# Optimization experiments

Measured on AMD Instinct MI355X. Metric: run time of the kernel, lower is better.

The kernel has to match this reference:

```python
import jax, jax.numpy as jnp
import numpy as np

RC = 6.0
N_BASIS = 32
WIDTH = 0.25
N_CONV = 3
MU = jnp.linspace(0.5, 6.0, N_BASIS)  # Gaussian RBF centers ('distances')


def ssp(x):
    # shifted softplus activation (SchNet-style)
    return jax.nn.softplus(x) - jnp.log(2.0)


def setup_inputs() -> dict:
    key = jax.random.key(0)
    ks = jax.random.split(key, 20)
    B, N, F, K = 16, 128, 128, 32
    S = 16  # n_species
    coords = jax.random.normal(ks[0], (B, N, 3), dtype=jnp.float32) * 4.0
    species = jax.random.randint(ks[1], (B, N), 0, S)
    g = lambda k, shape, fan: jax.random.normal(k, shape, dtype=jnp.float32) / np.sqrt(fan)
    return {
        "coords": coords,
        "species": species,
        "emb_table": g(ks[2], (S, F), 1.0),
        # convolve_net: K -> F -> F
        "Wc1": g(ks[3], (K, F), K), "bc1": jnp.zeros((F,)),
        "Wc2": g(ks[4], (F, F), F), "bc2": jnp.zeros((F,)),
        # update_net: F -> F -> F
        "Wu1": g(ks[5], (F, F), F), "bu1": jnp.zeros((F,)),
        "Wu2": g(ks[6], (F, F), F), "bu2": jnp.zeros((F,)),
        # pool_net: F -> 64 -> 8 (isotropic coefficients)
        "Wp1": g(ks[7], (F, 64), F), "bp1": jnp.zeros((64,)),
        "Wp2": g(ks[8], (64, 8), 64), "bp2": jnp.zeros((8,)),
        # edge_net: 2F -> F -> 16 (anisotropic coefficients); split as Wi/Wj
        "Wei": g(ks[9], (F, F), 2 * F), "Wej": g(ks[10], (F, F), 2 * F),
        "be1": jnp.zeros((F,)),
        "We2": g(ks[11], (F, 16), F), "be2": jnp.zeros((16,)),
    }


def reference(coords, species, emb_table,
              Wc1, bc1, Wc2, bc2,
              Wu1, bu1, Wu2, bu2,
              Wp1, bp1, Wp2, bp2,
              Wei, Wej, be1, We2, be2):
    B, N, _ = coords.shape
    # --- MolecularEmbedding ---
    h = emb_table[species]                                   # [B,N,F]
    # --- pairwise geometry (shared across conv iterations; coords fixed) ---
    diff = coords[:, :, None, :] - coords[:, None, :, :]      # [B,N,N,3]
    d2 = jnp.sum(diff * diff, axis=-1)                        # [B,N,N]
    d = jnp.sqrt(jnp.where(d2 > 0, d2, 1.0))                  # safe sqrt (diag masked out)
    eye = jnp.eye(N, dtype=bool)
    mask = ((d < RC) & ~eye).astype(h.dtype)[..., None]       # [B,N,N,1]
    rbf = jnp.exp(-((d[..., None] - MU) ** 2) / (2.0 * WIDTH ** 2))  # [B,N,N,K]
    # convolve_net: RBF -> continuous filter weights [B,N,N,F]
    Wf = (ssp(rbf @ Wc1 + bc1) @ Wc2 + bc2) * mask
    # --- n_convolutions x MessagePassing ---
    for _ in range(N_CONV):
        m = jnp.einsum('bijf,bjf->bif', Wf, h)                # gather-weight-scatter
        h = h + (ssp(m @ Wu1 + bu1) @ Wu2 + bu2)              # update_net (residual)
    # --- NodePool -> c_iso [B,N,8] ---
    c_iso = ssp(h @ Wp1 + bp1) @ Wp2 + bp2
    # --- EdgePool -> c_aniso [B,N,N,16], summed over neighbor axis ---
    pre_i = h @ Wei                                           # [B,N,F]
    pre_j = h @ Wej                                           # [B,N,F]
    hid = ssp(pre_i[:, :, None, :] + pre_j[:, None, :, :] + be1)  # [B,N,N,F]
    c_aniso = (hid @ We2 + be2) * mask                        # [B,N,N,16]
    return c_iso, c_aniso.sum(2)
```

## Files before the change

### kernel.cpp

```cpp
#include <hip/hip_runtime.h>


#define LN2F 0.69314718055994531f

__device__ __forceinline__ float sspf(float x) {
  float e = __expf(-fabsf(x));
  return fmaxf(x, 0.0f) + __logf(1.0f + e) - LN2F;
}
__device__ __forceinline__ unsigned int f2bf(float x) {
  unsigned int u = __float_as_uint(x);
  return (u + 0x7fffu + ((u >> 16) & 1u)) >> 16;
}
__device__ __forceinline__ float bflo(unsigned int u) { return __uint_as_float(u << 16); }
__device__ __forceinline__ float bfhi(unsigned int u) { return __uint_as_float(u & 0xffff0000u); }

__global__ __launch_bounds__(256) void prep_kernel(
    const float* __restrict__ coords,
    const float* __restrict__ Wc1, const float* __restrict__ bc1,
    const float* __restrict__ Wc2, const float* __restrict__ bc2,
    float* __restrict__ table,
    unsigned int* __restrict__ ent, int* __restrict__ cnt) {
  int t = threadIdx.x;
  if (blockIdx.x < 1024) {
    __shared__ int wc[4];
    int node = blockIdx.x * 2 + (t >> 7);
    int j = t & 127;
    int b = node >> 7, i = node & 127;
    const float* cb = coords + (b << 7) * 3;
    float dx = cb[i*3+0] - cb[j*3+0];
    float dy = cb[i*3+1] - cb[j*3+1];
    float dz = cb[i*3+2] - cb[j*3+2];
    float d  = sqrtf(dx*dx + dy*dy + dz*dz);
    bool valid = (d < 6.0f) && (j != i);
    int k = 4096;
    if (valid) { k = (int)(d * (4096.0f/6.0f)); if (k > 4095) k = 4095; }
    unsigned long long bal = __ballot(valid);
    int lane = t & 63, w = t >> 6;
    if (lane == 0) wc[w] = (int)__popcll(bal);
    __syncthreads();
    int ii = t >> 7;
    int nn = wc[2*ii] + wc[2*ii+1];
    int base = ((w & 1) ? wc[w-1] : 0) + (int)__popcll(bal & ((1ull << lane) - 1ull));
    if (valid) ent[node*128 + base] = (unsigned int)(j | (k << 7));
    int nnp = (nn + 3) & ~3;
    if (j >= nn && j < nnp) ent[node*128 + j] = (4096u << 7);
    if (j == 0) cnt[node] = nn | (nnp << 16);
  } else {
    __shared__ float rbf[8][32];
    __shared__ float hid[8][128];
    int tb = (int)blockIdx.x - 1024;
    int t0 = tb * 8;
    { int tt = t >> 5, kk = t & 31;
      float d = (float)(t0 + tt) * (6.0f/4096.0f) + 0.5f * (6.0f/4096.0f);
      float mu = 0.5f + (float)kk * (5.5f/31.0f);
      float z = d - mu;
      rbf[tt][kk] = __expf(-8.0f * z * z); }
    __syncthreads();
    int f = t & 127, sub = t >> 7;
    float s0 = bc1[f], s1 = s0, s2 = s0, s3 = s0;
    int r0 = sub * 4;
    for (int kk = 0; kk < 32; kk++) {
      float wv = Wc1[kk*128 + f];
      s0 += rbf[r0+0][kk]*wv; s1 += rbf[r0+1][kk]*wv;
      s2 += rbf[r0+2][kk]*wv; s3 += rbf[r0+3][kk]*wv;
    }
    hid[r0+0][f] = sspf(s0); hid[r0+1][f] = sspf(s1);
    hid[r0+2][f] = sspf(s2); hid[r0+3][f] = sspf(s3);
    __syncthreads();
    float o0 = bc2[f], o1 = o0, o2 = o0, o3 = o0;
    for (int g = 0; g < 128; g++) {
      float wv = Wc2[g*128 + f];
      o0 += hid[r0+0][g]*wv; o1 += hid[r0+1][g]*wv;
      o2 += hid[r0+2][g]*wv; o3 += hid[r0+3][g]*wv;
    }
    table[(t0+r0+0)*128 + f] = o0;
    table[(t0+r0+1)*128 + f] = o1;
    table[(t0+r0+2)*128 + f] = o2;
    table[(t0+r0+3)*128 + f] = o3;
    if (tb == 0 && t < 128) table[4096*128 + t] = 0.0f;
  }
}

template<bool SRC_EMB, bool LAST>
__global__ __launch_bounds__(512) void conv_t(
    const float* __restrict__ h_in, const unsigned int* __restrict__ hbf_in,
    float* __restrict__ h_out, unsigned int* __restrict__ hbf_out,
    const int* __restrict__ species, const float* __restrict__ emb,
    const float* __restrict__ table, const unsigned int* __restrict__ ent,
    const int* __restrict__ cnt,
    const float* __restrict__ Wu1, const float* __restrict__ bu1,
    const float* __restrict__ Wu2, const float* __restrict__ bu2,
    const float* __restrict__ Wp1, const float* __restrict__ bp1,
    const float* __restrict__ Wp2, const float* __restrict__ bp2,
    const float* __restrict__ Wei, const float* __restrict__ Wej,
    float* __restrict__ pre_i, unsigned int* __restrict__ prejbf,
    float* __restrict__ out) {
  __shared__ unsigned int hsh[8192];
  __shared__ unsigned int ent_s[4][128];
  __shared__ float mred[8][128];
  __shared__ float m_s[4][128];
  __shared__ float red[4][4][128];
  __shared__ float u1_s[4][128];
  __shared__ int nn_s[4];
  int t = threadIdx.x;
  int node0 = blockIdx.x * 4;
  int b = blockIdx.x >> 5;

  if constexpr (SRC_EMB) {
    const int* spb = species + (b << 7);
    for (int c = 0; c < 16; c++) {
      int idx = c*512 + t;
      int j = idx >> 6, f2 = idx & 63;
      float2 v = *(const float2*)(emb + spb[j]*128 + 2*f2);
      hsh[idx] = (f2bf(v.y) << 16) | f2bf(v.x);
    }
  } else {
    const unsigned int* hb = hbf_in + b * 8192;
    for (int c = 0; c < 16; c++) hsh[c*512 + t] = hb[c*512 + t];
  }
  { int ii = t >> 7, f = t & 127;
    ent_s[ii][f] = ent[(node0 + ii)*128 + f]; }
  if (t < 4) nn_s[t] = cnt[node0 + t];
  __syncthreads();

  int w = t >> 6, lane = t & 63;
  int ii = w >> 1, par = w & 1;
  int nnp = nn_s[ii] >> 16;
  float a0 = 0.f, a1 = 0.f, c0 = 0.f, c1 = 0.f;
  for (int e = par; e + 2 < nnp; e += 4) {
    unsigned int u0 = ent_s[ii][e], u1 = ent_s[ii][e + 2];
    int j0 = u0 & 127, k0 = (int)(u0 >> 7);
    int j1 = u1 & 127, k1 = (int)(u1 >> 7);
    float2 t0 = *(const float2*)(table + k0*128 + 2*lane);
    float2 t1 = *(const float2*)(table + k1*128 + 2*lane);
    unsigned int h0 = hsh[j0*64 + lane];
    unsigned int h1 = hsh[j1*64 + lane];
    a0 += t0.x * bflo(h0); a1 += t0.y * bfhi(h0);
    c0 += t1.x * bflo(h1); c1 += t1.y * bfhi(h1);
  }
  a0 += c0; a1 += c1;
  *(float2*)&mred[w][2*lane] = make_float2(a0, a1);
  __syncthreads();
  { int i2 = t >> 7, f = t & 127;
    m_s[i2][f] = mred[2*i2][f] + mred[2*i2+1][f]; }
  __syncthreads();

  int g = t & 127, q = t >> 7;
  {
    float p0=0,p1=0,p2=0,p3=0;
    for (int f = q*32; f < q*32 + 32; f++) {
      float wv = Wu1[f*128 + g];
      p0 += m_s[0][f]*wv; p1 += m_s[1][f]*wv; p2 += m_s[2][f]*wv; p3 += m_s[3][f]*wv;
    }
    red[q][0][g]=p0; red[q][1][g]=p1; red[q][2][g]=p2; red[q][3][g]=p3;
  }
  __syncthreads();
  { int i2 = t >> 7, gg = t & 127;
    u1_s[i2][gg] = sspf(red[0][i2][gg]+red[1][i2][gg]+red[2][i2][gg]+red[3][i2][gg] + bu1[gg]); }
  __syncthreads();
  {
    float p0=0,p1=0,p2=0,p3=0;
    for (int f = q*32; f < q*32 + 32; f++) {
      float wv = Wu2[f*128 + g];
      p0 += u1_s[0][f]*wv; p1 += u1_s[1][f]*wv; p2 += u1_s[2][f]*wv; p3 += u1_s[3][f]*wv;
    }
    red[q][0][g]=p0; red[q][1][g]=p1; red[q][2][g]=p2; red[q][3][g]=p3;
  }
  __syncthreads();
  { int i2 = t >> 7, o = t & 127;
    int node = node0 + i2;
    float delta = red[0][i2][o]+red[1][i2][o]+red[2][i2][o]+red[3][i2][o] + bu2[o];
    float base;
    if constexpr (SRC_EMB) base = emb[species[node]*128 + o];
    else                   base = h_in[node*128 + o];
    float hf = base + delta;
    if constexpr (!LAST) {
      h_out[node*128 + o] = hf;
      unsigned int lo = f2bf(hf);
      unsigned int hi = (unsigned int)__shfl_xor((int)lo, 1);
      if ((o & 1) == 0) hbf_out[node*64 + (o >> 1)] = lo | (hi << 16);
    } else {
      u1_s[i2][o] = hf;
    }
  }
  if constexpr (LAST) {
    __syncthreads();
    float (*hs)[128]     = u1_s;
    float (*redp)[4][64] = reinterpret_cast<float (*)[4][64]>(red);
    float (*us)[64]      = reinterpret_cast<float (*)[64]>(m_s);
    int gp = t & 63, qp = t >> 6;
    float p0=0,p1=0,p2=0,p3=0;
    for (int f = qp*16; f < qp*16 + 16; f++) {
      float wv = Wp1[f*64 + gp];
      p0 += hs[0][f]*wv; p1 += hs[1][f]*wv; p2 += hs[2][f]*wv; p3 += hs[3][f]*wv;
    }
    redp[qp][0][gp]=p0; redp[qp][1][gp]=p1; redp[qp][2][gp]=p2; redp[qp][3][gp]=p3;
    __syncthreads();
    if (t < 256) {
      int i4 = t >> 6, gg = t & 63;
      float s = bp1[gg];
      for (int q2 = 0; q2 < 8; q2++) s += redp[q2][i4][gg];
      us[i4][gg] = sspf(s);
    }
    __syncthreads();
    if (t < 32) {
      int i4 = t >> 3, o = t & 7;
      float v = bp2[o];
      for (int gg = 0; gg < 64; gg++) v += us[i4][gg] * Wp2[gg*8 + o];
      out[(node0 + i4)*8 + o] = v;
    }
    int o = t & 127, sel = (t >> 7) & 1, duo = t >> 8;
    const float* W = sel ? Wej : Wei;
    float q0 = 0.f, q1 = 0.f;
    for (int f = 0; f < 128; f++) {
      float wv = W[f*128 + o];
      q0 += hs[2*duo][f]*wv; q1 += hs[2*duo+1][f]*wv;
    }
    if (sel == 0) {
      pre_i[(node0 + 2*duo)*128 + o]     = q0;
      pre_i[(node0 + 2*duo + 1)*128 + o] = q1;
    } else {
      unsigned int l0 = f2bf(q0), l1 = f2bf(q1);
      unsigned int h0 = (unsigned int)__shfl_xor((int)l0, 1);
      unsigned int h1 = (unsigned int)__shfl_xor((int)l1, 1);
      if ((o & 1) == 0) {
        prejbf[(node0 + 2*duo)*64 + (o >> 1)]     = l0 | (h0 << 16);
        prejbf[(node0 + 2*duo + 1)*64 + (o >> 1)] = l1 | (h1 << 16);
      }
    }
  }
}

__global__ __launch_bounds__(512) void edgepool_kernel(
    const float* __restrict__ pre_i, const unsigned int* __restrict__ prejbf,
    const unsigned int* __restrict__ ent, const int* __restrict__ cnt,
    const float* __restrict__ be1, const float* __restrict__ We2,
    const float* __restrict__ be2, float* __restrict__ out) {
  __shared__ unsigned int pjs[8192];
  __shared__ unsigned int ent_s[4][128];
  __shared__ float pis[4][128];
  __shared__ float sred[8][128];
  __shared__ float s_s[4][128];
  __shared__ float r2[4][8][16];
  __shared__ int nn_s[4];
  int t = threadIdx.x;
  int node0 = blockIdx.x * 4;
  int b = blockIdx.x >> 5;
  const unsigned int* pjb = prejbf + b * 8192;
  for (int c = 0; c < 16; c++) pjs[c*512 + t] = pjb[c*512 + t];
  { int ii = t >> 7, f = t & 127;
    pis[ii][f] = pre_i[(node0 + ii)*128 + f] + be1[f];
    ent_s[ii][f] = ent[(node0 + ii)*128 + f]; }
  if (t < 4) nn_s[t] = cnt[node0 + t] & 0xffff;
  __syncthreads();
  int w = t >> 6, lane = t & 63;
  int ii = w >> 1, par = w & 1;
  float pia = pis[ii][2*lane];
  float pib = pis[ii][2*lane + 1];
  int nn = nn_s[ii];
  float a0 = 0.f, a1 = 0.f;
  for (int e = par; e < nn; e += 2) {
    unsigned int u = ent_s[ii][e];
    int j = u & 127;
    unsigned int hv = pjs[j*64 + lane];
    a0 += sspf(pia + bflo(hv));
    a1 += sspf(pib + bfhi(hv));
  }
  *(float2*)&sred[w][2*lane] = make_float2(a0, a1);
  __syncthreads();
  { int i2 = t >> 7, f = t & 127;
    s_s[i2][f] = sred[2*i2][f] + sred[2*i2+1][f]; }
  __syncthreads();
  { int i2 = t >> 7, o = t & 15, seg = (t >> 4) & 7;
    float p = 0.f;
    for (int f = seg*16; f < seg*16 + 16; f++) p += s_s[i2][f] * We2[f*16 + o];
    r2[i2][seg][o] = p; }
  __syncthreads();
  if (t < 64) {
    int i2 = t >> 4, o = t & 15;
    float v = be2[o] * (float)nn_s[i2];
    for (int seg = 0; seg < 8; seg++) v += r2[i2][seg][o];
    out[(node0 + i2)*16 + o] = v;
  }
}

extern "C" void kernel_launch(void* const* d_in, const int* in_sizes, int n_in,
                              void* d_out, int out_size, void* d_ws, size_t ws_size,
                              hipStream_t stream) {
  const float* coords = (const float*)d_in[0];
  const int*   species= (const int*)  d_in[1];
  const float* emb    = (const float*)d_in[2];
  const float* Wc1    = (const float*)d_in[3];
  const float* bc1    = (const float*)d_in[4];
  const float* Wc2    = (const float*)d_in[5];
  const float* bc2    = (const float*)d_in[6];
  const float* Wu1    = (const float*)d_in[7];
  const float* bu1    = (const float*)d_in[8];
  const float* Wu2    = (const float*)d_in[9];
  const float* bu2    = (const float*)d_in[10];
  const float* Wp1    = (const float*)d_in[11];
  const float* bp1    = (const float*)d_in[12];
  const float* Wp2    = (const float*)d_in[13];
  const float* bp2    = (const float*)d_in[14];
  const float* Wei    = (const float*)d_in[15];
  const float* Wej    = (const float*)d_in[16];
  const float* be1    = (const float*)d_in[17];
  const float* We2    = (const float*)d_in[18];
  const float* be2    = (const float*)d_in[19];
  float* out = (float*)d_out;

  float* wsf = (float*)d_ws;
  float*        table  = wsf;
  float*        h_a    = wsf + 524416;
  float*        h_b    = wsf + 786560;
  float*        pre_i  = wsf + 1048704;
  unsigned int* hbf_a  = (unsigned int*)(wsf + 1310848);
  unsigned int* hbf_b  = (unsigned int*)(wsf + 1441920);
  unsigned int* prejbf = (unsigned int*)(wsf + 1572992);
  unsigned int* ent    = (unsigned int*)(wsf + 1704064);
  int*          cnt    = (int*)(wsf + 1966208);
  (void)in_sizes; (void)n_in; (void)out_size; (void)ws_size;

  prep_kernel<<<1536, 256, 0, stream>>>(coords, Wc1, bc1, Wc2, bc2, table, ent, cnt);
  conv_t<true, false><<<512, 512, 0, stream>>>(
      nullptr, nullptr, h_b, hbf_b, species, emb, table, ent, cnt,
      Wu1, bu1, Wu2, bu2,
      nullptr, nullptr, nullptr, nullptr, nullptr, nullptr, nullptr, nullptr, nullptr);
  conv_t<false, false><<<512, 512, 0, stream>>>(
      h_b, hbf_b, h_a, hbf_a, species, emb, table, ent, cnt,
      Wu1, bu1, Wu2, bu2,
      nullptr, nullptr, nullptr, nullptr, nullptr, nullptr, nullptr, nullptr, nullptr);
  conv_t<false, true><<<512, 512, 0, stream>>>(
      h_a, hbf_a, nullptr, nullptr, species, emb, table, ent, cnt,
      Wu1, bu1, Wu2, bu2,
      Wp1, bp1, Wp2, bp2, Wei, Wej, pre_i, prejbf, out);
  edgepool_kernel<<<512, 512, 0, stream>>>(pre_i, prejbf, ent, cnt, be1, We2, be2,
                                           out + 16384);
}
```

Baseline: 60.05 us.

## Merge prep branches, unroll gather loop 4-way, vectorize smem staging, drop reduction barriers

Each prep block now builds both a neighbor list and a slice of the filter table: 1024 blocks handling 4 table rows each, where before 1536 blocks were split by role. Neighbor padding grows to a multiple of 8 so the conv gather loop can run four independent accumulators. Shared-memory staging of h and pre_j uses 128-bit loads, the emb staging uses float4. The separate pairwise-sum passes and their barriers in the conv and edgepool kernels are folded into the following matmul loops, and several inner loops get unroll pragmas. The trade is more padded zero entries per row and more redundant adds inside the matmul loops.

Result: slower. 75.82 us (+26.3%).

```diff
diff --git a/kernel.cpp b/kernel.cpp
--- a/kernel.cpp
+++ b/kernel.cpp
@@ -20,10 +20,14 @@
     const float* __restrict__ Wc2, const float* __restrict__ bc2,
     float* __restrict__ table,
     unsigned int* __restrict__ ent, int* __restrict__ cnt) {
+  __shared__ int wc[4];
+  __shared__ float rbf[4][32];
+  __shared__ float hid[4][128];
   int t = threadIdx.x;
-  if (blockIdx.x < 1024) {
-    __shared__ int wc[4];
-    int node = blockIdx.x * 2 + (t >> 7);
+  int blk = blockIdx.x;
+
+  {
+    int node = blk * 2 + (t >> 7);
     int j = t & 127;
     int b = node >> 7, i = node & 127;
     const float* cb = coords + (b << 7) * 3;
@@ -42,42 +46,40 @@
     int nn = wc[2*ii] + wc[2*ii+1];
     int base = ((w & 1) ? wc[w-1] : 0) + (int)__popcll(bal & ((1ull << lane) - 1ull));
     if (valid) ent[node*128 + base] = (unsigned int)(j | (k << 7));
-    int nnp = (nn + 3) & ~3;
+    int nnp = (nn + 7) & ~7;
+    if (nnp > 128) nnp = 128;
     if (j >= nn && j < nnp) ent[node*128 + j] = (4096u << 7);
     if (j == 0) cnt[node] = nn | (nnp << 16);
-  } else {
-    __shared__ float rbf[8][32];
-    __shared__ float hid[8][128];
-    int tb = (int)blockIdx.x - 1024;
-    int t0 = tb * 8;
-    { int tt = t >> 5, kk = t & 31;
-      float d = (float)(t0 + tt) * (6.0f/4096.0f) + 0.5f * (6.0f/4096.0f);
+  }
+  {
+    int r0 = blk * 4;
+    if (t < 128) {
+      int tt = t >> 5, kk = t & 31;
+      float d = (float)(r0 + tt) * (6.0f/4096.0f) + 0.5f * (6.0f/4096.0f);
       float mu = 0.5f + (float)kk * (5.5f/31.0f);
       float z = d - mu;
-      rbf[tt][kk] = __expf(-8.0f * z * z); }
+      rbf[tt][kk] = __expf(-8.0f * z * z);
+    }
     __syncthreads();
     int f = t & 127, sub = t >> 7;
-    float s0 = bc1[f], s1 = s0, s2 = s0, s3 = s0;
-    int r0 = sub * 4;
+    int ra = sub*2, rb = ra + 1;
+    float s0 = bc1[f], s1 = s0;
+#pragma unroll 8
     for (int kk = 0; kk < 32; kk++) {
       float wv = Wc1[kk*128 + f];
-      s0 += rbf[r0+0][kk]*wv; s1 += rbf[r0+1][kk]*wv;
-      s2 += rbf[r0+2][kk]*wv; s3 += rbf[r0+3][kk]*wv;
-    }
-    hid[r0+0][f] = sspf(s0); hid[r0+1][f] = sspf(s1);
-    hid[r0+2][f] = sspf(s2); hid[r0+3][f] = sspf(s3);
-    __syncthreads();
-    float o0 = bc2[f], o1 = o0, o2 = o0, o3 = o0;
+      s0 += rbf[ra][kk]*wv; s1 += rbf[rb][kk]*wv;
+    }
+    hid[ra][f] = sspf(s0); hid[rb][f] = sspf(s1);
+    __syncthreads();
+    float o0 = bc2[f], o1 = o0;
+#pragma unroll 8
     for (int g = 0; g < 128; g++) {
       float wv = Wc2[g*128 + f];
-      o0 += hid[r0+0][g]*wv; o1 += hid[r0+1][g]*wv;
-      o2 += hid[r0+2][g]*wv; o3 += hid[r0+3][g]*wv;
-    }
-    table[(t0+r0+0)*128 + f] = o0;
-    table[(t0+r0+1)*128 + f] = o1;
-    table[(t0+r0+2)*128 + f] = o2;
-    table[(t0+r0+3)*128 + f] = o3;
-    if (tb == 0 && t < 128) table[4096*128 + t] = 0.0f;
+      o0 += hid[ra][g]*wv; o1 += hid[rb][g]*wv;
+    }
+    table[(r0+ra)*128 + f] = o0;
+    table[(r0+rb)*128 + f] = o1;
+    if (blk == 0 && t < 128) table[4096*128 + t] = 0.0f;
   }
 }
 
@@ -98,7 +100,7 @@
   __shared__ unsigned int hsh[8192];
   __shared__ unsigned int ent_s[4][128];
   __shared__ float mred[8][128];
-  __shared__ float m_s[4][128];
+  __shared__ float scr[4][128];
   __shared__ float red[4][4][128];
   __shared__ float u1_s[4][128];
   __shared__ int nn_s[4];
@@ -108,15 +110,20 @@
 
   if constexpr (SRC_EMB) {
     const int* spb = species + (b << 7);
-    for (int c = 0; c < 16; c++) {
+    const float4* emb4 = (const float4*)emb;
+    for (int c = 0; c < 8; c++) {
       int idx = c*512 + t;
-      int j = idx >> 6, f2 = idx & 63;
-      float2 v = *(const float2*)(emb + spb[j]*128 + 2*f2);
-      hsh[idx] = (f2bf(v.y) << 16) | f2bf(v.x);
+      int j = idx >> 5, f4 = idx & 31;
+      float4 v = emb4[spb[j]*32 + f4];
+      uint2 pk;
+      pk.x = (f2bf(v.y) << 16) | f2bf(v.x);
+      pk.y = (f2bf(v.w) << 16) | f2bf(v.z);
+      ((uint2*)hsh)[j*32 + f4] = pk;
     }
   } else {
-    const unsigned int* hb = hbf_in + b * 8192;
-    for (int c = 0; c < 16; c++) hsh[c*512 + t] = hb[c*512 + t];
+    const uint4* hb4 = (const uint4*)(hbf_in + b * 8192);
+    uint4* hsh4 = (uint4*)hsh;
+    for (int c = 0; c < 4; c++) hsh4[c*512 + t] = hb4[c*512 + t];
   }
   { int ii = t >> 7, f = t & 127;
     ent_s[ii][f] = ent[(node0 + ii)*128 + f]; }
@@ -126,31 +133,36 @@
   int w = t >> 6, lane = t & 63;
   int ii = w >> 1, par = w & 1;
   int nnp = nn_s[ii] >> 16;
-  float a0 = 0.f, a1 = 0.f, c0 = 0.f, c1 = 0.f;
-  for (int e = par; e + 2 < nnp; e += 4) {
-    unsigned int u0 = ent_s[ii][e], u1 = ent_s[ii][e + 2];
-    int j0 = u0 & 127, k0 = (int)(u0 >> 7);
-    int j1 = u1 & 127, k1 = (int)(u1 >> 7);
-    float2 t0 = *(const float2*)(table + k0*128 + 2*lane);
-    float2 t1 = *(const float2*)(table + k1*128 + 2*lane);
-    unsigned int h0 = hsh[j0*64 + lane];
-    unsigned int h1 = hsh[j1*64 + lane];
+  float a0 = 0.f, a1 = 0.f, b0 = 0.f, b1 = 0.f;
+  float c0 = 0.f, c1 = 0.f, d0 = 0.f, d1 = 0.f;
+  for (int e = par; e < nnp; e += 8) {
+    unsigned int u0 = ent_s[ii][e],     u1 = ent_s[ii][e + 2];
+    unsigned int u2 = ent_s[ii][e + 4], u3 = ent_s[ii][e + 6];
+    float2 t0 = *(const float2*)(table + (u0 >> 7)*128 + 2*lane);
+    float2 t1 = *(const float2*)(table + (u1 >> 7)*128 + 2*lane);
+    float2 t2 = *(const float2*)(table + (u2 >> 7)*128 + 2*lane);
+    float2 t3 = *(const float2*)(table + (u3 >> 7)*128 + 2*lane);
+    unsigned int h0 = hsh[(u0 & 127)*64 + lane];
+    unsigned int h1 = hsh[(u1 & 127)*64 + lane];
+    unsigned int h2 = hsh[(u2 & 127)*64 + lane];
+    unsigned int h3 = hsh[(u3 & 127)*64 + lane];
     a0 += t0.x * bflo(h0); a1 += t0.y * bfhi(h0);
-    c0 += t1.x * bflo(h1); c1 += t1.y * bfhi(h1);
-  }
-  a0 += c0; a1 += c1;
+    b0 += t1.x * bflo(h1); b1 += t1.y * bfhi(h1);
+    c0 += t2.x * bflo(h2); c1 += t2.y * bfhi(h2);
+    d0 += t3.x * bflo(h3); d1 += t3.y * bfhi(h3);
+  }
+  a0 += b0 + c0 + d0; a1 += b1 + c1 + d1;
   *(float2*)&mred[w][2*lane] = make_float2(a0, a1);
-  __syncthreads();
-  { int i2 = t >> 7, f = t & 127;
-    m_s[i2][f] = mred[2*i2][f] + mred[2*i2+1][f]; }
   __syncthreads();
 
   int g = t & 127, q = t >> 7;
   {
     float p0=0,p1=0,p2=0,p3=0;
+#pragma unroll 8
     for (int f = q*32; f < q*32 + 32; f++) {
       float wv = Wu1[f*128 + g];
-      p0 += m_s[0][f]*wv; p1 += m_s[1][f]*wv; p2 += m_s[2][f]*wv; p3 += m_s[3][f]*wv;
+      p0 += (mred[0][f]+mred[1][f])*wv; p1 += (mred[2][f]+mred[3][f])*wv;
+      p2 += (mred[4][f]+mred[5][f])*wv; p3 += (mred[6][f]+mred[7][f])*wv;
     }
     red[q][0][g]=p0; red[q][1][g]=p1; red[q][2][g]=p2; red[q][3][g]=p3;
   }
@@ -160,6 +172,7 @@
   __syncthreads();
   {
     float p0=0,p1=0,p2=0,p3=0;
+#pragma unroll 8
     for (int f = q*32; f < q*32 + 32; f++) {
       float wv = Wu2[f*128 + g];
       p0 += u1_s[0][f]*wv; p1 += u1_s[1][f]*wv; p2 += u1_s[2][f]*wv; p3 += u1_s[3][f]*wv;
@@ -187,9 +200,10 @@
     __syncthreads();
     float (*hs)[128]     = u1_s;
     float (*redp)[4][64] = reinterpret_cast<float (*)[4][64]>(red);
-    float (*us)[64]      = reinterpret_cast<float (*)[64]>(m_s);
+    float (*us)[64]      = reinterpret_cast<float (*)[64]>(scr);
     int gp = t & 63, qp = t >> 6;
     float p0=0,p1=0,p2=0,p3=0;
+#pragma unroll 8
     for (int f = qp*16; f < qp*16 + 16; f++) {
       float wv = Wp1[f*64 + gp];
       p0 += hs[0][f]*wv; p1 += hs[1][f]*wv; p2 += hs[2][f]*wv; p3 += hs[3][f]*wv;
@@ -199,6 +213,7 @@
     if (t < 256) {
       int i4 = t >> 6, gg = t & 63;
       float s = bp1[gg];
+#pragma unroll
       for (int q2 = 0; q2 < 8; q2++) s += redp[q2][i4][gg];
       us[i4][gg] = sspf(s);
     }
@@ -206,12 +221,14 @@
     if (t < 32) {
       int i4 = t >> 3, o = t & 7;
       float v = bp2[o];
+#pragma unroll 8
       for (int gg = 0; gg < 64; gg++) v += us[i4][gg] * Wp2[gg*8 + o];
       out[(node0 + i4)*8 + o] = v;
     }
     int o = t & 127, sel = (t >> 7) & 1, duo = t >> 8;
     const float* W = sel ? Wej : Wei;
     float q0 = 0.f, q1 = 0.f;
+#pragma unroll 8
     for (int f = 0; f < 128; f++) {
       float wv = W[f*128 + o];
       q0 += hs[2*duo][f]*wv; q1 += hs[2*duo+1][f]*wv;
@@ -240,14 +257,14 @@
   __shared__ unsigned int ent_s[4][128];
   __shared__ float pis[4][128];
   __shared__ float sred[8][128];
-  __shared__ float s_s[4][128];
   __shared__ float r2[4][8][16];
   __shared__ int nn_s[4];
   int t = threadIdx.x;
   int node0 = blockIdx.x * 4;
   int b = blockIdx.x >> 5;
-  const unsigned int* pjb = prejbf + b * 8192;
-  for (int c = 0; c < 16; c++) pjs[c*512 + t] = pjb[c*512 + t];
+  { const uint4* pjb4 = (const uint4*)(prejbf + b * 8192);
+    uint4* pjs4 = (uint4*)pjs;
+    for (int c = 0; c < 4; c++) pjs4[c*512 + t] = pjb4[c*512 + t]; }
   { int ii = t >> 7, f = t & 127;
     pis[ii][f] = pre_i[(node0 + ii)*128 + f] + be1[f];
     ent_s[ii][f] = ent[(node0 + ii)*128 + f]; }
@@ -268,17 +285,17 @@
   }
   *(float2*)&sred[w][2*lane] = make_float2(a0, a1);
   __syncthreads();
-  { int i2 = t >> 7, f = t & 127;
-    s_s[i2][f] = sred[2*i2][f] + sred[2*i2+1][f]; }
-  __syncthreads();
   { int i2 = t >> 7, o = t & 15, seg = (t >> 4) & 7;
     float p = 0.f;
-    for (int f = seg*16; f < seg*16 + 16; f++) p += s_s[i2][f] * We2[f*16 + o];
+#pragma unroll
+    for (int f = seg*16; f < seg*16 + 16; f++)
+      p += (sred[2*i2][f] + sred[2*i2+1][f]) * We2[f*16 + o];
     r2[i2][seg][o] = p; }
   __syncthreads();
   if (t < 64) {
     int i2 = t >> 4, o = t & 15;
     float v = be2[o] * (float)nn_s[i2];
+#pragma unroll
     for (int seg = 0; seg < 8; seg++) v += r2[i2][seg][o];
     out[(node0 + i2)*16 + o] = v;
   }
@@ -321,7 +338,7 @@
   int*          cnt    = (int*)(wsf + 1966208);
   (void)in_sizes; (void)n_in; (void)out_size; (void)ws_size;
 
-  prep_kernel<<<1536, 256, 0, stream>>>(coords, Wc1, bc1, Wc2, bc2, table, ent, cnt);
+  prep_kernel<<<1024, 256, 0, stream>>>(coords, Wc1, bc1, Wc2, bc2, table, ent, cnt);
   conv_t<true, false><<<512, 512, 0, stream>>>(
       nullptr, nullptr, h_b, hbf_b, species, emb, table, ent, cnt,
       Wu1, bu1, Wu2, bu2,
```
